# Kernel tuning notes

Measured on AMD Instinct MI355X. Metric: run time of the kernel, lower is better.

## Reference

```python
import jax, jax.numpy as jnp
import numpy as np

# Residue-type multiplicative bonuses from _add_chemical_property_bonuses
# dict: {1:1.3, 3:1.2, 6:1.2, 8:1.4, 11:1.3, 13:1.5, 17:1.6, 18:1.4, 19:1.1,
#        0:1.05, 2:1.1, 5:1.1, 15:1.05, 16:1.05}, default 1.0
_BOND_TABLE = np.full(20, 1.0, dtype=np.float32)
for k, v in {1: 1.3, 3: 1.2, 6: 1.2, 8: 1.4, 11: 1.3, 13: 1.5, 17: 1.6,
             18: 1.4, 19: 1.1, 0: 1.05, 2: 1.1, 5: 1.1, 15: 1.05, 16: 1.05}.items():
    _BOND_TABLE[k] = v

DIRECT_R = 3.5    # direct contact radius (A)
EXT_R = 8.0       # extended interaction radius (A)
NEIGH_R2 = 25.0   # surface-accessibility neighbor radius squared (5 A)^2


def setup_inputs() -> dict:
    key = jax.random.key(0)
    k1, k2, k3, k4 = jax.random.split(key, 4)
    N, M, F = 16384, 64, 16
    pos = jax.random.uniform(k1, (N, 3), dtype=jnp.float32) * 40.0          # protein box
    ligand_pos = jax.random.uniform(k2, (M, 3), dtype=jnp.float32) * 10.0 + 15.0  # centered ligand
    x = jax.random.normal(k3, (N, F), dtype=jnp.float32)
    res = jax.random.randint(k4, (N,), 0, 20)
    x = x.at[:, 1].set(res.astype(jnp.float32))  # column 1 = residue type code
    return {"pos": pos, "ligand_pos": ligand_pos, "x": x, "max_atoms": 512}


def reference(pos, ligand_pos, x, max_atoms):
    # --- min distance of each pocket atom to any ligand atom: [N]
    d2l_sq = jnp.sum((pos[:, None, :] - ligand_pos[None, :, :]) ** 2, axis=-1)  # [N, M]
    min_d = jnp.sqrt(jnp.maximum(jnp.min(d2l_sq, axis=1), 1e-12))               # [N]

    direct = min_d <= DIRECT_R
    extended = (min_d > DIRECT_R) & (min_d <= EXT_R)
    far = min_d > EXT_R

    # --- surface accessibility among far atoms only (as in torch: pos[far_mask])
    # Compare squared distances (equivalent to d<5 & d>0, avoids sqrt on the NxN block).
    sq = jnp.sum((pos[:, None, :] - pos[None, :, :]) ** 2, axis=-1)  # [N, N]
    neigh = (sq < NEIGH_R2) & (sq > 0.0) & far[None, :]              # neighbors within far subset
    counts = jnp.where(far, jnp.sum(neigh, axis=1).astype(pos.dtype), 0.0)
    max_n = jnp.max(counts)
    max_n = jnp.where(max_n > 0, max_n, 1.0)
    surface = 1.0 - counts / (max_n + 1e-6)

    # --- tiered scores
    scores = jnp.where(
        direct, 10.0,
        jnp.where(extended, 5.0 * (EXT_R - min_d) / EXT_R, surface))

    # --- chemical property bonuses (vectorized lookup-table gather)
    res_type = jnp.clip(x[:, 1].astype(jnp.int32), 0, 19)
    scores = scores * jnp.asarray(_BOND_TABLE)[res_type]

    top_scores, indices = jax.lax.top_k(scores, max_atoms)
    return scores, top_scores, indices
```

## Files before the change

kernel.cpp:

```cpp
#include <hip/hip_runtime.h>
#include <stdint.h>

#define TILE 256

__device__ __constant__ float BOND[20] = {
    1.05f, 1.30f, 1.10f, 1.20f, 1.00f, 1.10f, 1.20f, 1.00f, 1.40f, 1.00f,
    1.00f, 1.30f, 1.00f, 1.50f, 1.00f, 1.05f, 1.05f, 1.60f, 1.40f, 1.10f};

__global__ void k_init(int* __restrict__ counts, int* __restrict__ rankv,
                       int* __restrict__ maxn, int N) {
  int i = blockIdx.x * blockDim.x + threadIdx.x;
  if (i < N) { counts[i] = 0; rankv[i] = 0; }
  if (i == 0) *maxn = 0;
}

__global__ void k_classify(const float* __restrict__ pos, const float* __restrict__ lig,
                           float* __restrict__ min_d, float4* __restrict__ posj,
                           int N, int M) {
#pragma clang fp contract(off)
  __shared__ float sl[3 * 256];
  int t = threadIdx.x;
  for (int idx = t; idx < M * 3; idx += blockDim.x) sl[idx] = lig[idx];
  __syncthreads();
  int i = blockIdx.x * blockDim.x + t;
  if (i >= N) return;
  float px = pos[3 * i], py = pos[3 * i + 1], pz = pos[3 * i + 2];
  float m = 3.4e38f;
  for (int j = 0; j < M; ++j) {
    float dx = px - sl[3 * j];
    float dy = py - sl[3 * j + 1];
    float dz = pz - sl[3 * j + 2];
    float d2 = dx * dx + dy * dy + dz * dz;
    m = fminf(m, d2);
  }
  float md = sqrtf(fmaxf(m, 1e-12f));
  min_d[i] = md;
  bool far = md > 8.0f;
  posj[i] = make_float4(far ? px : 3.0e30f, py, pz, 0.0f);
}

__global__ void k_count(const float* __restrict__ pos, const float4* __restrict__ posj,
                        int* __restrict__ counts, int N, int jChunk) {
#pragma clang fp contract(off)
  __shared__ float4 sj[TILE];
  int t = threadIdx.x;
  int i = blockIdx.x * TILE + t;
  bool valid = i < N;
  int ii = valid ? i : 0;
  float px = pos[3 * ii], py = pos[3 * ii + 1], pz = pos[3 * ii + 2];
  int j0 = blockIdx.y * jChunk;
  int j1 = j0 + jChunk;
  if (j1 > N) j1 = N;
  int cnt = 0;
  for (int jb = j0; jb < j1; jb += TILE) {
    __syncthreads();
    if (jb + t < N) sj[t] = posj[jb + t];
    else            sj[t] = make_float4(3.0e30f, 0.f, 0.f, 0.f);
    __syncthreads();
#pragma unroll 16
    for (int jj = 0; jj < TILE; ++jj) {
      float4 q = sj[jj];
      float dx = px - q.x;
      float dy = py - q.y;
      float dz = pz - q.z;
      float d2 = dx * dx + dy * dy + dz * dz;
      cnt += (d2 < 25.0f && d2 > 0.0f) ? 1 : 0;
    }
  }
  if (valid && cnt) atomicAdd(&counts[i], cnt);
}

__global__ void k_max(const int* __restrict__ counts, const float* __restrict__ min_d,
                      int* __restrict__ maxn, int N) {
  int i = blockIdx.x * blockDim.x + threadIdx.x;
  int c = 0;
  if (i < N && min_d[i] > 8.0f) c = counts[i];
  for (int off = 32; off > 0; off >>= 1) {
    int o = __shfl_down(c, off, 64);
    c = c > o ? c : o;
  }
  if ((threadIdx.x & 63) == 0) atomicMax(maxn, c);
}

__global__ void k_score(const float* __restrict__ min_d, const int* __restrict__ counts,
                        const int* __restrict__ maxn, const float* __restrict__ x,
                        float* __restrict__ out_scores, uint64_t* __restrict__ keys,
                        int N, int F) {
#pragma clang fp contract(off)
  int i = blockIdx.x * blockDim.x + threadIdx.x;
  if (i >= N) return;
  float md = min_d[i];
  float mn = (float)(*maxn);
  if (!(mn > 0.0f)) mn = 1.0f;
  float score;
  if (md <= 3.5f) {
    score = 10.0f;
  } else if (md <= 8.0f) {
    score = 5.0f * (8.0f - md) / 8.0f;
  } else {
    float cf = (float)counts[i];
    score = 1.0f - cf / (mn + 1e-6f);
  }
  int rt = (int)x[(size_t)i * F + 1];
  rt = rt < 0 ? 0 : (rt > 19 ? 19 : rt);
  score = score * BOND[rt];
  out_scores[i] = score;
  uint32_t fb = __float_as_uint(score);
  keys[i] = ((uint64_t)fb << 32) | (uint64_t)(0x7FFFFFFFu - (uint32_t)i);
}

__global__ void k_rank(const uint64_t* __restrict__ keys, int* __restrict__ rankv,
                       int N, int jChunk) {
  __shared__ uint64_t sk[TILE];
  int t = threadIdx.x;
  int i = blockIdx.x * TILE + t;
  bool valid = i < N;
  uint64_t ki = valid ? keys[i] : ~0ull;
  int j0 = blockIdx.y * jChunk;
  int j1 = j0 + jChunk;
  if (j1 > N) j1 = N;
  int r = 0;
  for (int jb = j0; jb < j1; jb += TILE) {
    __syncthreads();
    sk[t] = (jb + t < N) ? keys[jb + t] : 0ull;
    __syncthreads();
#pragma unroll 16
    for (int jj = 0; jj < TILE; ++jj) r += (sk[jj] > ki) ? 1 : 0;
  }
  if (valid && r) atomicAdd(&rankv[i], r);
}

__global__ void k_emit(const int* __restrict__ rankv, const float* __restrict__ scores,
                       float* __restrict__ top_scores, float* __restrict__ top_idx,
                       int N, int K) {
  int i = blockIdx.x * blockDim.x + threadIdx.x;
  if (i >= N) return;
  int r = rankv[i];
  if (r < K) {
    top_scores[r] = scores[i];
    top_idx[r] = (float)i;
  }
}

extern "C" void kernel_launch(void* const* d_in, const int* in_sizes, int n_in,
                              void* d_out, int out_size, void* d_ws, size_t ws_size,
                              hipStream_t stream) {
  const float* pos = (const float*)d_in[0];
  const float* lig = (const float*)d_in[1];
  const float* x   = (const float*)d_in[2];
  int N = in_sizes[0] / 3;
  int M = in_sizes[1] / 3;
  int F = in_sizes[2] / N;
  int K = (out_size - N) / 2;

  char* ws = (char*)d_ws;
  float4*   posj   = (float4*)ws;
  uint64_t* keys   = (uint64_t*)(ws + (size_t)N * 16);
  float*    min_d  = (float*)(ws + (size_t)N * 24);
  int*      counts = (int*)(ws + (size_t)N * 28);
  int*      rankv  = (int*)(ws + (size_t)N * 32);
  int*      maxn   = (int*)(ws + (size_t)N * 36);

  float* out_scores = (float*)d_out;
  float* out_top    = out_scores + N;
  float* out_idx    = out_top + K;

  int nb = (N + TILE - 1) / TILE;
  const int JSPLIT = 16;
  int jChunk = (N + JSPLIT - 1) / JSPLIT;
  jChunk = ((jChunk + TILE - 1) / TILE) * TILE;

  hipLaunchKernelGGL(k_init,     dim3(nb), dim3(TILE), 0, stream, counts, rankv, maxn, N);
  hipLaunchKernelGGL(k_classify, dim3(nb), dim3(TILE), 0, stream, pos, lig, min_d, posj, N, M);
  hipLaunchKernelGGL(k_count,    dim3(nb, JSPLIT), dim3(TILE), 0, stream, pos, posj, counts, N, jChunk);
  hipLaunchKernelGGL(k_max,      dim3(nb), dim3(TILE), 0, stream, counts, min_d, maxn, N);
  hipLaunchKernelGGL(k_score,    dim3(nb), dim3(TILE), 0, stream, min_d, counts, maxn, x, out_scores, keys, N, F);
  hipLaunchKernelGGL(k_rank,     dim3(nb, JSPLIT), dim3(TILE), 0, stream, keys, rankv, N, jChunk);
  hipLaunchKernelGGL(k_emit,     dim3(nb), dim3(TILE), 0, stream, rankv, out_scores, out_top, out_idx, N, K);
}
```

Measured before the change: 168.4 us.

## Replace all-pairs neighbor count and rank top-k with grid search and histogram selection

```diff
diff --git a/kernel.cpp b/kernel.cpp
--- a/kernel.cpp
+++ b/kernel.cpp
@@ -2,25 +2,31 @@
 #include <stdint.h>
 
 #define TILE 256
+#define NCELLS 512
+#define NHIST 2048
 
 __device__ __constant__ float BOND[20] = {
     1.05f, 1.30f, 1.10f, 1.20f, 1.00f, 1.10f, 1.20f, 1.00f, 1.40f, 1.00f,
     1.00f, 1.30f, 1.00f, 1.50f, 1.00f, 1.05f, 1.05f, 1.60f, 1.40f, 1.10f};
 
-__global__ void k_init(int* __restrict__ counts, int* __restrict__ rankv,
-                       int* __restrict__ maxn, int N) {
-  int i = blockIdx.x * blockDim.x + threadIdx.x;
-  if (i < N) { counts[i] = 0; rankv[i] = 0; }
-  if (i == 0) *maxn = 0;
+__device__ __forceinline__ int clamp8(int v) { return v < 0 ? 0 : (v > 7 ? 7 : v); }
+
+__global__ void k_init(int* __restrict__ cellCount, int* __restrict__ hist,
+                       int* __restrict__ scalars) {
+  int t = blockIdx.x * blockDim.x + threadIdx.x;
+  int stride = blockDim.x * gridDim.x;
+  for (int b = t; b < NCELLS; b += stride) cellCount[b] = 0;
+  for (int b = t; b < NHIST; b += stride) hist[b] = 0;
+  if (t < 4) scalars[t] = 0;
 }
 
 __global__ void k_classify(const float* __restrict__ pos, const float* __restrict__ lig,
-                           float* __restrict__ min_d, float4* __restrict__ posj,
+                           float* __restrict__ minD, int* __restrict__ cellCount,
                            int N, int M) {
 #pragma clang fp contract(off)
-  __shared__ float sl[3 * 256];
-  int t = threadIdx.x;
-  for (int idx = t; idx < M * 3; idx += blockDim.x) sl[idx] = lig[idx];
+  __shared__ float sl[768];
+  int t = threadIdx.x;
+  for (int idx = t; idx < 3 * M; idx += blockDim.x) sl[idx] = lig[idx];
   __syncthreads();
   int i = blockIdx.x * blockDim.x + t;
   if (i >= N) return;
@@ -34,111 +40,187 @@
     m = fminf(m, d2);
   }
   float md = sqrtf(fmaxf(m, 1e-12f));
-  min_d[i] = md;
-  bool far = md > 8.0f;
-  posj[i] = make_float4(far ? px : 3.0e30f, py, pz, 0.0f);
-}
-
-__global__ void k_count(const float* __restrict__ pos, const float4* __restrict__ posj,
-                        int* __restrict__ counts, int N, int jChunk) {
+  minD[i] = md;
+  if (md > 8.0f) {
+    int cx = clamp8((int)(px * 0.2f));
+    int cy = clamp8((int)(py * 0.2f));
+    int cz = clamp8((int)(pz * 0.2f));
+    atomicAdd(&cellCount[(cz * 8 + cy) * 8 + cx], 1);
+  }
+}
+
+__global__ void k_scan(const int* __restrict__ cellCount, int* __restrict__ cellStart,
+                       int* __restrict__ cellCursor) {
+  __shared__ int s[256];
+  int t = threadIdx.x;
+  int c0 = cellCount[2 * t], c1 = cellCount[2 * t + 1];
+  int p = c0 + c1;
+  s[t] = p;
+  __syncthreads();
+  for (int off = 1; off < 256; off <<= 1) {
+    int v = (t >= off) ? s[t - off] : 0;
+    __syncthreads();
+    s[t] += v;
+    __syncthreads();
+  }
+  int excl = s[t] - p;
+  cellStart[2 * t] = excl;          cellCursor[2 * t] = excl;
+  cellStart[2 * t + 1] = excl + c0; cellCursor[2 * t + 1] = excl + c0;
+  if (t == 255) cellStart[NCELLS] = s[255];
+}
+
+__global__ void k_scatter(const float* __restrict__ pos, const float* __restrict__ minD,
+                          int* __restrict__ cellCursor, float4* __restrict__ sortedPos,
+                          int N) {
+  int i = blockIdx.x * blockDim.x + threadIdx.x;
+  if (i >= N) return;
+  if (!(minD[i] > 8.0f)) return;
+  float px = pos[3 * i], py = pos[3 * i + 1], pz = pos[3 * i + 2];
+  int cx = clamp8((int)(px * 0.2f));
+  int cy = clamp8((int)(py * 0.2f));
+  int cz = clamp8((int)(pz * 0.2f));
+  int slot = atomicAdd(&cellCursor[(cz * 8 + cy) * 8 + cx], 1);
+  sortedPos[slot] = make_float4(px, py, pz, __int_as_float(i));
+}
+
+__global__ void k_query(const float4* __restrict__ sortedPos,
+                        const int* __restrict__ cellStart, int* __restrict__ counts,
+                        int* __restrict__ scalars, int N) {
 #pragma clang fp contract(off)
-  __shared__ float4 sj[TILE];
-  int t = threadIdx.x;
-  int i = blockIdx.x * TILE + t;
-  bool valid = i < N;
-  int ii = valid ? i : 0;
-  float px = pos[3 * ii], py = pos[3 * ii + 1], pz = pos[3 * ii + 2];
-  int j0 = blockIdx.y * jChunk;
-  int j1 = j0 + jChunk;
-  if (j1 > N) j1 = N;
+  int t = blockIdx.x * blockDim.x + threadIdx.x;
+  int F = cellStart[NCELLS];
   int cnt = 0;
-  for (int jb = j0; jb < j1; jb += TILE) {
-    __syncthreads();
-    if (jb + t < N) sj[t] = posj[jb + t];
-    else            sj[t] = make_float4(3.0e30f, 0.f, 0.f, 0.f);
-    __syncthreads();
-#pragma unroll 16
-    for (int jj = 0; jj < TILE; ++jj) {
-      float4 q = sj[jj];
-      float dx = px - q.x;
-      float dy = py - q.y;
-      float dz = pz - q.z;
-      float d2 = dx * dx + dy * dy + dz * dz;
-      cnt += (d2 < 25.0f && d2 > 0.0f) ? 1 : 0;
+  if (t < F) {
+    float4 q = sortedPos[t];
+    int cx = clamp8((int)(q.x * 0.2f));
+    int cy = clamp8((int)(q.y * 0.2f));
+    int cz = clamp8((int)(q.z * 0.2f));
+    int x0 = cx > 0 ? cx - 1 : 0;
+    int x1 = cx < 7 ? cx + 1 : 7;
+    int zlo = cz > 0 ? cz - 1 : 0, zhi = cz < 7 ? cz + 1 : 7;
+    int ylo = cy > 0 ? cy - 1 : 0, yhi = cy < 7 ? cy + 1 : 7;
+    for (int z = zlo; z <= zhi; ++z) {
+      for (int y = ylo; y <= yhi; ++y) {
+        int rb = (z * 8 + y) * 8;
+        int k0 = cellStart[rb + x0];
+        int k1 = cellStart[rb + x1 + 1];
+        for (int k = k0; k < k1; ++k) {
+          float4 p = sortedPos[k];
+          float dx = q.x - p.x;
+          float dy = q.y - p.y;
+          float dz = q.z - p.z;
+          float d2 = dx * dx + dy * dy + dz * dz;
+          cnt += (d2 < 25.0f && d2 > 0.0f) ? 1 : 0;
+        }
+      }
     }
-  }
-  if (valid && cnt) atomicAdd(&counts[i], cnt);
-}
-
-__global__ void k_max(const int* __restrict__ counts, const float* __restrict__ min_d,
-                      int* __restrict__ maxn, int N) {
-  int i = blockIdx.x * blockDim.x + threadIdx.x;
-  int c = 0;
-  if (i < N && min_d[i] > 8.0f) c = counts[i];
+    counts[__float_as_int(q.w)] = cnt;
+  }
+  int c = cnt;
   for (int off = 32; off > 0; off >>= 1) {
     int o = __shfl_down(c, off, 64);
     c = c > o ? c : o;
   }
-  if ((threadIdx.x & 63) == 0) atomicMax(maxn, c);
-}
-
-__global__ void k_score(const float* __restrict__ min_d, const int* __restrict__ counts,
-                        const int* __restrict__ maxn, const float* __restrict__ x,
+  if ((threadIdx.x & 63) == 0 && c > 0) atomicMax(&scalars[0], c);
+}
+
+__global__ void k_score(const float* __restrict__ minD, const int* __restrict__ counts,
+                        const int* __restrict__ scalars, const float* __restrict__ x,
                         float* __restrict__ out_scores, uint64_t* __restrict__ keys,
-                        int N, int F) {
+                        int* __restrict__ hist, int N, int F) {
 #pragma clang fp contract(off)
+  __shared__ int lh[NHIST];
+  for (int b = threadIdx.x; b < NHIST; b += blockDim.x) lh[b] = 0;
+  __syncthreads();
+  int i = blockIdx.x * blockDim.x + threadIdx.x;
+  if (i < N) {
+    float md = minD[i];
+    float mn = (float)scalars[0];
+    if (!(mn > 0.0f)) mn = 1.0f;
+    float score;
+    if (md <= 3.5f) {
+      score = 10.0f;
+    } else if (md <= 8.0f) {
+      score = 5.0f * (8.0f - md) / 8.0f;
+    } else {
+      float cf = (float)counts[i];
+      score = 1.0f - cf / (mn + 1e-6f);
+    }
+    int rt = (int)x[(size_t)i * F + 1];
+    rt = rt < 0 ? 0 : (rt > 19 ? 19 : rt);
+    score = score * BOND[rt];
+    out_scores[i] = score;
+    uint32_t fb = __float_as_uint(score);
+    keys[i] = ((uint64_t)fb << 32) | (uint64_t)(0x7FFFFFFFu - (uint32_t)i);
+    atomicAdd(&lh[fb >> 20], 1);
+  }
+  __syncthreads();
+  for (int b = threadIdx.x; b < NHIST; b += blockDim.x) {
+    int v = lh[b];
+    if (v) atomicAdd(&hist[b], v);
+  }
+}
+
+__global__ void k_sel(const int* __restrict__ hist, int* __restrict__ scalars, int K) {
+  __shared__ int s[256];
+  int t = threadIdx.x;
+  int base = t * 8;
+  int local = 0;
+  for (int b = 0; b < 8; ++b) local += hist[base + b];
+  s[t] = local;
+  __syncthreads();
+  for (int off = 1; off < 256; off <<= 1) {
+    int v = (t + off < 256) ? s[t + off] : 0;
+    __syncthreads();
+    s[t] += v;
+    __syncthreads();
+  }
+  int cumNext = (t < 255) ? s[t + 1] : 0;
+  if (s[t] >= K && cumNext < K) {
+    int running = cumNext;
+    int B = base;
+    for (int b = base + 7; b >= base; --b) {
+      running += hist[b];
+      if (running >= K) { B = b; break; }
+    }
+    scalars[2] = B;
+  }
+}
+
+__global__ void k_compact(const uint64_t* __restrict__ keys, int* __restrict__ scalars,
+                          uint64_t* __restrict__ cand, int N) {
   int i = blockIdx.x * blockDim.x + threadIdx.x;
   if (i >= N) return;
-  float md = min_d[i];
-  float mn = (float)(*maxn);
-  if (!(mn > 0.0f)) mn = 1.0f;
-  float score;
-  if (md <= 3.5f) {
-    score = 10.0f;
-  } else if (md <= 8.0f) {
-    score = 5.0f * (8.0f - md) / 8.0f;
-  } else {
-    float cf = (float)counts[i];
-    score = 1.0f - cf / (mn + 1e-6f);
-  }
-  int rt = (int)x[(size_t)i * F + 1];
-  rt = rt < 0 ? 0 : (rt > 19 ? 19 : rt);
-  score = score * BOND[rt];
-  out_scores[i] = score;
-  uint32_t fb = __float_as_uint(score);
-  keys[i] = ((uint64_t)fb << 32) | (uint64_t)(0x7FFFFFFFu - (uint32_t)i);
-}
-
-__global__ void k_rank(const uint64_t* __restrict__ keys, int* __restrict__ rankv,
-                       int N, int jChunk) {
+  uint64_t k = keys[i];
+  if ((int)(k >> 52) >= scalars[2]) {
+    int p = atomicAdd(&scalars[1], 1);
+    cand[p] = k;
+  }
+}
+
+__global__ void k_rank_emit(const uint64_t* __restrict__ cand,
+                            const int* __restrict__ scalars,
+                            float* __restrict__ out_top, float* __restrict__ out_idx,
+                            int K) {
+  int C = scalars[1];
+  if (blockIdx.x * blockDim.x >= C) return;
   __shared__ uint64_t sk[TILE];
   int t = threadIdx.x;
-  int i = blockIdx.x * TILE + t;
-  bool valid = i < N;
-  uint64_t ki = valid ? keys[i] : ~0ull;
-  int j0 = blockIdx.y * jChunk;
-  int j1 = j0 + jChunk;
-  if (j1 > N) j1 = N;
+  int g = blockIdx.x * blockDim.x + t;
+  uint64_t ki = (g < C) ? cand[g] : ~0ull;
   int r = 0;
-  for (int jb = j0; jb < j1; jb += TILE) {
-    __syncthreads();
-    sk[t] = (jb + t < N) ? keys[jb + t] : 0ull;
+  int nt = (C + TILE - 1) / TILE;
+  for (int tb = 0; tb < nt; ++tb) {
+    __syncthreads();
+    int j = tb * TILE + t;
+    sk[t] = (j < C) ? cand[j] : 0ull;
     __syncthreads();
 #pragma unroll 16
     for (int jj = 0; jj < TILE; ++jj) r += (sk[jj] > ki) ? 1 : 0;
   }
-  if (valid && r) atomicAdd(&rankv[i], r);
-}
-
-__global__ void k_emit(const int* __restrict__ rankv, const float* __restrict__ scores,
-                       float* __restrict__ top_scores, float* __restrict__ top_idx,
-                       int N, int K) {
-  int i = blockIdx.x * blockDim.x + threadIdx.x;
-  if (i >= N) return;
-  int r = rankv[i];
-  if (r < K) {
-    top_scores[r] = scores[i];
-    top_idx[r] = (float)i;
+  if (g < C && r < K) {
+    out_top[r] = __uint_as_float((uint32_t)(ki >> 32));
+    out_idx[r] = (float)(0x7FFFFFFFu - (uint32_t)ki);
   }
 }
 
@@ -154,27 +236,31 @@
   int K = (out_size - N) / 2;
 
   char* ws = (char*)d_ws;
-  float4*   posj   = (float4*)ws;
-  uint64_t* keys   = (uint64_t*)(ws + (size_t)N * 16);
-  float*    min_d  = (float*)(ws + (size_t)N * 24);
-  int*      counts = (int*)(ws + (size_t)N * 28);
-  int*      rankv  = (int*)(ws + (size_t)N * 32);
-  int*      maxn   = (int*)(ws + (size_t)N * 36);
+  size_t off = 0;
+  float4*   sortedPos = (float4*)(ws + off);   off += (size_t)N * 16;
+  uint64_t* keys      = (uint64_t*)(ws + off); off += (size_t)N * 8;
+  float*    minD      = (float*)(ws + off);    off += (size_t)N * 4;
+  int*      counts    = (int*)(ws + off);      off += (size_t)N * 4;
+  int*      cellCount = (int*)(ws + off);      off += (size_t)NCELLS * 4;
+  int*      cellStart = (int*)(ws + off);      off += (size_t)(NCELLS + 1) * 4;
+  int*      cellCursor= (int*)(ws + off);      off += (size_t)NCELLS * 4;
+  int*      hist      = (int*)(ws + off);      off += (size_t)NHIST * 4;
+  int*      scalars   = (int*)(ws + off);      off += 16;
+  uint64_t* cand      = (uint64_t*)sortedPos;
 
   float* out_scores = (float*)d_out;
   float* out_top    = out_scores + N;
   float* out_idx    = out_top + K;
 
   int nb = (N + TILE - 1) / TILE;
-  const int JSPLIT = 16;
-  int jChunk = (N + JSPLIT - 1) / JSPLIT;
-  jChunk = ((jChunk + TILE - 1) / TILE) * TILE;
-
-  hipLaunchKernelGGL(k_init,     dim3(nb), dim3(TILE), 0, stream, counts, rankv, maxn, N);
-  hipLaunchKernelGGL(k_classify, dim3(nb), dim3(TILE), 0, stream, pos, lig, min_d, posj, N, M);
-  hipLaunchKernelGGL(k_count,    dim3(nb, JSPLIT), dim3(TILE), 0, stream, pos, posj, counts, N, jChunk);
-  hipLaunchKernelGGL(k_max,      dim3(nb), dim3(TILE), 0, stream, counts, min_d, maxn, N);
-  hipLaunchKernelGGL(k_score,    dim3(nb), dim3(TILE), 0, stream, min_d, counts, maxn, x, out_scores, keys, N, F);
-  hipLaunchKernelGGL(k_rank,     dim3(nb, JSPLIT), dim3(TILE), 0, stream, keys, rankv, N, jChunk);
-  hipLaunchKernelGGL(k_emit,     dim3(nb), dim3(TILE), 0, stream, rankv, out_scores, out_top, out_idx, N, K);
-}
+
+  hipLaunchKernelGGL(k_init,     dim3(4),  dim3(TILE), 0, stream, cellCount, hist, scalars);
+  hipLaunchKernelGGL(k_classify, dim3(nb), dim3(TILE), 0, stream, pos, lig, minD, cellCount, N, M);
+  hipLaunchKernelGGL(k_scan,     dim3(1),  dim3(TILE), 0, stream, cellCount, cellStart, cellCursor);
+  hipLaunchKernelGGL(k_scatter,  dim3(nb), dim3(TILE), 0, stream, pos, minD, cellCursor, sortedPos, N);
+  hipLaunchKernelGGL(k_query,    dim3(nb), dim3(TILE), 0, stream, sortedPos, cellStart, counts, scalars, N);
+  hipLaunchKernelGGL(k_score,    dim3(nb), dim3(TILE), 0, stream, minD, counts, scalars, x, out_scores, keys, hist, N, F);
+  hipLaunchKernelGGL(k_sel,      dim3(1),  dim3(TILE), 0, stream, hist, scalars, K);
+  hipLaunchKernelGGL(k_compact,  dim3(nb), dim3(TILE), 0, stream, keys, scalars, cand, N);
+  hipLaunchKernelGGL(k_rank_emit,dim3(nb), dim3(TILE), 0, stream, cand, scalars, out_top, out_idx, K);
+}
```

Measured after the change: 192.8 us. 1.14x slower.
